# Kernel tuning notes

Hardware: AMD Instinct MI355X
Metric: run time of the kernel (lower is better)

## Reference

```python
import jax, jax.numpy as jnp
import numpy as np

BATCH, FEAT, N_IN, N_OUT = 2, 16, 2048, 4096  # nodes=N_IN, hyperedges=N_OUT
AVG_INCIDENCE = 3.0  # avg nodes per hyperedge


def setup_inputs() -> dict:
    key = jax.random.key(0)
    kx, kb = jax.random.split(key)
    x = jax.random.normal(kx, (BATCH, FEAT, N_IN), dtype=jnp.float32)
    # Bt = incidenceMatrix.T, shape [n_out_nodes, n_in_nodes], binary {0,1}
    Bt = (jax.random.uniform(kb, (N_OUT, N_IN)) < (AVG_INCIDENCE / N_IN)).astype(jnp.float32)
    return {"x": x, "Bt": Bt}


def reference(x, Bt):
    # Faithful to PoolCliqueToLine.forward:
    #   v[b, c, m] = max_n x[b, c, n] * Bt[m, n]
    # The torch code loops over batch and 8-feature chunks doing the same dense
    # broadcast-multiply + max; here it is fully vectorized in one expression.
    # Note: because Bt is mostly zero, the dense max implicitly clamps at 0
    # (x * 0 terms participate in the max), exactly as in the original.
    # intermediate: [B, C, M, N]
    return jnp.max(x[:, :, None, :] * Bt[None, None, :, :], axis=-1)
```

## Files before the change

kernel.cpp:

```cpp
#include <hip/hip_runtime.h>


#define HG_N_IN   2048
#define HG_N_OUT  4096
#define HG_BC     32

__global__ __launch_bounds__(256) void hg_rowmax(const float4* __restrict__ Bt4,
                                                 const float* __restrict__ x,
                                                 float* __restrict__ out) {
    __shared__ unsigned short idx[HG_N_IN];
    __shared__ int lds_cnt;
    const int m = blockIdx.x;
    const int t = threadIdx.x;
    if (t == 0) lds_cnt = 0;
    __syncthreads();

    const float4* row = Bt4 + (size_t)m * (HG_N_IN / 4);
    #pragma unroll
    for (int c = 0; c < 2; ++c) {
        const int v4 = t + c * 256;
        const float4 v = row[v4];
        const int n0 = v4 << 2;
        if (v.x != 0.0f) idx[atomicAdd(&lds_cnt, 1)] = (unsigned short)(n0);
        if (v.y != 0.0f) idx[atomicAdd(&lds_cnt, 1)] = (unsigned short)(n0 + 1);
        if (v.z != 0.0f) idx[atomicAdd(&lds_cnt, 1)] = (unsigned short)(n0 + 2);
        if (v.w != 0.0f) idx[atomicAdd(&lds_cnt, 1)] = (unsigned short)(n0 + 3);
    }
    __syncthreads();

    const int cnt = lds_cnt;
    if (t < HG_BC) {
        const float* xr = x + (size_t)t * HG_N_IN;
        float mx = (cnt == HG_N_IN) ? -INFINITY : 0.0f;
        for (int k = 0; k < cnt; ++k) {
            mx = fmaxf(mx, xr[idx[k]]);
        }
        out[(size_t)t * HG_N_OUT + m] = mx;
    }
}

extern "C" void kernel_launch(void* const* d_in, const int* in_sizes, int n_in,
                              void* d_out, int out_size, void* d_ws, size_t ws_size,
                              hipStream_t stream) {
    const float* x    = (const float*)d_in[0];
    const float4* Bt4 = (const float4*)d_in[1];
    float* out = (float*)d_out;

    hg_rowmax<<<HG_N_OUT, 256, 0, stream>>>(Bt4, x, out);
}
```

Baseline: 12.91 us.

## Assign one wavefront per hyperedge row using ballot-based nonzero compaction

Each 64-lane wavefront now handles one output row instead of a 256-thread block per row. Nonzeros are located with wave ballots and shuffles instead of LDS atomics, so shared memory and both block barriers go away. Four rows share a block, which cuts the grid size. In exchange, each lane holds eight float4 loads in registers, and the nonzero walk runs serially across the wave.

```diff
diff --git a/kernel.cpp b/kernel.cpp
--- a/kernel.cpp
+++ b/kernel.cpp
@@ -8,34 +8,43 @@
 __global__ __launch_bounds__(256) void hg_rowmax(const float4* __restrict__ Bt4,
                                                  const float* __restrict__ x,
                                                  float* __restrict__ out) {
-    __shared__ unsigned short idx[HG_N_IN];
-    __shared__ int lds_cnt;
-    const int m = blockIdx.x;
-    const int t = threadIdx.x;
-    if (t == 0) lds_cnt = 0;
-    __syncthreads();
+    const int wavesPerBlk = blockDim.x >> 6;
+    const int m    = blockIdx.x * wavesPerBlk + (threadIdx.x >> 6);
+    const int lane = threadIdx.x & 63;
+    if (m >= HG_N_OUT) return;
 
     const float4* row = Bt4 + (size_t)m * (HG_N_IN / 4);
+    float4 v[8];
     #pragma unroll
-    for (int c = 0; c < 2; ++c) {
-        const int v4 = t + c * 256;
-        const float4 v = row[v4];
-        const int n0 = v4 << 2;
-        if (v.x != 0.0f) idx[atomicAdd(&lds_cnt, 1)] = (unsigned short)(n0);
-        if (v.y != 0.0f) idx[atomicAdd(&lds_cnt, 1)] = (unsigned short)(n0 + 1);
-        if (v.z != 0.0f) idx[atomicAdd(&lds_cnt, 1)] = (unsigned short)(n0 + 2);
-        if (v.w != 0.0f) idx[atomicAdd(&lds_cnt, 1)] = (unsigned short)(n0 + 3);
+    for (int i = 0; i < 8; ++i) v[i] = row[lane + (i << 6)];
+
+    const float* xr = x + (size_t)(lane & (HG_BC - 1)) * HG_N_IN;
+    float mx = -INFINITY;
+    int cnt = 0;
+
+    #pragma unroll
+    for (int i = 0; i < 8; ++i) {
+        int code = (v[i].x != 0.0f) | ((v[i].y != 0.0f) << 1) |
+                   ((v[i].z != 0.0f) << 2) | ((v[i].w != 0.0f) << 3);
+        unsigned long long b = __ballot(code != 0);
+        if (b == 0ull) continue;
+        while (b) {
+            int s = __ffsll((unsigned long long)b) - 1;
+            b &= b - 1;
+            int c = __shfl(code, s);
+            int nbase = (s + (i << 6)) << 2;
+            while (c) {
+                int j = __ffs(c) - 1;
+                c &= c - 1;
+                ++cnt;
+                if (lane < HG_BC) mx = fmaxf(mx, xr[nbase + j]);
+            }
+        }
     }
-    __syncthreads();
 
-    const int cnt = lds_cnt;
-    if (t < HG_BC) {
-        const float* xr = x + (size_t)t * HG_N_IN;
-        float mx = (cnt == HG_N_IN) ? -INFINITY : 0.0f;
-        for (int k = 0; k < cnt; ++k) {
-            mx = fmaxf(mx, xr[idx[k]]);
-        }
-        out[(size_t)t * HG_N_OUT + m] = mx;
+    if (lane < HG_BC) {
+        float r = (cnt == HG_N_IN) ? mx : fmaxf(mx, 0.0f);
+        out[(size_t)lane * HG_N_OUT + m] = r;
     }
 }
 
@@ -46,5 +55,5 @@
     const float4* Bt4 = (const float4*)d_in[1];
     float* out = (float*)d_out;
 
-    hg_rowmax<<<HG_N_OUT, 256, 0, stream>>>(Bt4, x, out);
+    hg_rowmax<<<HG_N_OUT / 4, 256, 0, stream>>>(Bt4, x, out);
 }
```

After: 13.03 us. Within noise of the previous version (+0.9%).
